# Kernel optimization log

Measured on AMD Instinct MI355X. Metric: run time of the kernel, lower is better.

Reference implementation:

```python
import jax, jax.numpy as jnp
import numpy as np


def setup_inputs() -> dict:
    key = jax.random.key(0)
    ks = jax.random.split(key, 8)
    N, C, H, W = 4, 128, 64, 64
    x = jax.random.normal(ks[0], (N, C, H, W), dtype=jnp.float32)
    s = 1.0 / np.sqrt(C)
    wq = jax.random.normal(ks[1], (C, C), dtype=jnp.float32) * s
    bq = jax.random.normal(ks[2], (C,), dtype=jnp.float32) * 0.01
    wk = jax.random.normal(ks[3], (C, C), dtype=jnp.float32) * s
    bk = jax.random.normal(ks[4], (C,), dtype=jnp.float32) * 0.01
    wv = jax.random.normal(ks[5], (C, C), dtype=jnp.float32) * s
    bv = jax.random.normal(ks[6], (C,), dtype=jnp.float32) * 0.01
    gamma = jax.random.normal(ks[7], (1,), dtype=jnp.float32) * 0.1
    return {"x": x, "wq": wq, "bq": bq, "wk": wk, "bk": bk,
            "wv": wv, "bv": bv, "gamma": gamma}


def reference(x, wq, bq, wk, bk, wv, bv, gamma):
    N, C, H, W = x.shape
    xf = x.reshape(N, C, H * W)                      # [N, C, HW]
    # 1x1 convs == per-pixel channel GEMMs
    q = jnp.einsum('dc,nci->ndi', wq, xf) + bq[None, :, None]  # [N, C, HW]
    k = jnp.einsum('dc,nci->ndi', wk, xf) + bk[None, :, None]
    v = jnp.einsum('dc,nci->ndi', wv, xf) + bv[None, :, None]
    # scores[n,i,j] = sum_c q[n,c,i] * k[n,c,j]  (query^T @ key)
    scores = jnp.einsum('nci,ncj->nij', q, k)        # [N, HW, HW]
    attn = jax.nn.softmax(scores, axis=-1)
    # out[n,c,i] = sum_j v[n,c,j] * attn[n,i,j]  (value @ attn^T)
    out = jnp.einsum('ncj,nij->nci', v, attn).reshape(N, C, H, W)
    return gamma[0] * out + x
```

## Files before the change

kernel.cpp:

```cpp
#include <hip/hip_runtime.h>

#define HW 4096
#define CC 128
#define NB 4
#define NSPLIT 4
#define KEYS_PER_SPLIT (HW / NSPLIT)

typedef __bf16 bf16x8 __attribute__((ext_vector_type(8)));
typedef float floatx4 __attribute__((ext_vector_type(4)));

__device__ __forceinline__ float row_max16(float v) {
    int x;
    x = __builtin_amdgcn_update_dpp(0, __float_as_int(v), 0x128, 0xf, 0xf, false);
    v = fmaxf(v, __int_as_float(x));
    x = __builtin_amdgcn_update_dpp(0, __float_as_int(v), 0x124, 0xf, 0xf, false);
    v = fmaxf(v, __int_as_float(x));
    x = __builtin_amdgcn_update_dpp(0, __float_as_int(v), 0x122, 0xf, 0xf, false);
    v = fmaxf(v, __int_as_float(x));
    x = __builtin_amdgcn_update_dpp(0, __float_as_int(v), 0x121, 0xf, 0xf, false);
    v = fmaxf(v, __int_as_float(x));
    return v;
}
__device__ __forceinline__ float row_sum16(float v) {
    int x;
    x = __builtin_amdgcn_update_dpp(0, __float_as_int(v), 0x128, 0xf, 0xf, false);
    v += __int_as_float(x);
    x = __builtin_amdgcn_update_dpp(0, __float_as_int(v), 0x124, 0xf, 0xf, false);
    v += __int_as_float(x);
    x = __builtin_amdgcn_update_dpp(0, __float_as_int(v), 0x122, 0xf, 0xf, false);
    v += __int_as_float(x);
    x = __builtin_amdgcn_update_dpp(0, __float_as_int(v), 0x121, 0xf, 0xf, false);
    v += __int_as_float(x);
    return v;
}

__global__ __launch_bounds__(256) void wconv_kernel(
    const float* __restrict__ wq, const float* __restrict__ wk,
    const float* __restrict__ wv, __bf16* __restrict__ wb)
{
    int idx = blockIdx.x * 256 + threadIdx.x;
    int which = idx >> 14;
    int within = idx & 16383;
    const float* src = (which == 0) ? wq : (which == 1) ? wk : wv;
    wb[idx] = (__bf16)src[within];
}

__global__ __launch_bounds__(256) void proj_kernel(
    const float* __restrict__ x, const __bf16* __restrict__ wb,
    const float* __restrict__ bq, const float* __restrict__ bk,
    const float* __restrict__ bv,
    __bf16* __restrict__ qb, __bf16* __restrict__ kb, __bf16* __restrict__ vb)
{
    __shared__ char smem_raw[128 * 70 * 2];
    __bf16* Xt = reinterpret_cast<__bf16*>(smem_raw);
    __bf16* Vt = reinterpret_cast<__bf16*>(smem_raw);

    const int m   = blockIdx.x % 3;
    const int nit = blockIdx.x / 3;
    const int n   = nit >> 6;
    const int i0  = (nit & 63) << 6;
    const int t   = threadIdx.x;

    const float* xb = x + (size_t)n * CC * HW;

#pragma unroll 4
    for (int p = 0; p < 32; ++p) {
        int c  = p * 4 + (t >> 6);
        int il = t & 63;
        Xt[il * 136 + c] = (__bf16)xb[(size_t)c * HW + i0 + il];
    }
    __syncthreads();

    const int w    = t >> 6;
    const int lane = t & 63;
    const int l16  = lane & 15;
    const int quad = lane >> 4;

    bf16x8 afrag[4];
#pragma unroll
    for (int ks = 0; ks < 4; ++ks)
        afrag[ks] = *reinterpret_cast<const bf16x8*>(
            &Xt[(w * 16 + l16) * 136 + ks * 32 + quad * 8]);

    const __bf16* wm = wb + (size_t)m * CC * CC;
    const float* Bm = (m == 0) ? bq : (m == 1) ? bk : bv;

    if (m < 2) {
        __bf16* dst = (m == 0) ? qb : kb;
#pragma unroll
        for (int h = 0; h < 8; ++h) {
            int d = h * 16 + l16;
            floatx4 acc = {0.f, 0.f, 0.f, 0.f};
#pragma unroll
            for (int ks = 0; ks < 4; ++ks) {
                bf16x8 bfrag = *reinterpret_cast<const bf16x8*>(
                    wm + (size_t)d * CC + ks * 32 + quad * 8);
                acc = __builtin_amdgcn_mfma_f32_16x16x32_bf16(afrag[ks], bfrag, acc, 0, 0, 0);
            }
            float bias = Bm[d];
#pragma unroll
            for (int r = 0; r < 4; ++r) {
                int i = i0 + w * 16 + quad * 4 + r;
                dst[(size_t)n * HW * CC + (size_t)i * CC + d] = (__bf16)(acc[r] + bias);
            }
        }
    } else {
        __syncthreads();
#pragma unroll
        for (int h = 0; h < 8; ++h) {
            int d = h * 16 + l16;
            floatx4 acc = {0.f, 0.f, 0.f, 0.f};
#pragma unroll
            for (int ks = 0; ks < 4; ++ks) {
                bf16x8 bfrag = *reinterpret_cast<const bf16x8*>(
                    wm + (size_t)d * CC + ks * 32 + quad * 8);
                acc = __builtin_amdgcn_mfma_f32_16x16x32_bf16(afrag[ks], bfrag, acc, 0, 0, 0);
            }
            float bias = Bm[d];
#pragma unroll
            for (int r = 0; r < 4; ++r)
                Vt[d * 70 + w * 16 + quad * 4 + r] = (__bf16)(acc[r] + bias);
        }
        __syncthreads();
#pragma unroll 4
        for (int p = 0; p < 32; ++p) {
            int d  = p * 4 + (t >> 6);
            int il = t & 63;
            vb[((size_t)n * CC + d) * HW + i0 + il] = Vt[d * 70 + il];
        }
    }
}

#define KT_STRIDE 136
#define VT_STRIDE 72
#define PT_STRIDE 72
#define KT_BYTES (64 * KT_STRIDE * 2)
#define VT_BYTES (128 * VT_STRIDE * 2)
#define P_OFF    (KT_BYTES + VT_BYTES)
#define T_STRIDE 129

__global__ __launch_bounds__(256, 2) void attn_split_kernel(
    const __bf16* __restrict__ qb, const __bf16* __restrict__ kb,
    const __bf16* __restrict__ vb,
    float* __restrict__ opart, float* __restrict__ ml)
{
    __shared__ char smem[P_OFF + 4 * 32 * PT_STRIDE * 2];
    __bf16* Kt = reinterpret_cast<__bf16*>(smem);
    __bf16* Vt = reinterpret_cast<__bf16*>(smem + KT_BYTES);
    float*  T  = reinterpret_cast<float*>(smem);

    const int b     = blockIdx.x;
    const int n     = (b >> 1) & 3;
    const int split = (((b >> 3) & 1) << 1) | (b & 1);
    const int it    = b >> 4;
    const int i0    = it << 7;
    const int t     = threadIdx.x;
    const int w     = t >> 6;
    const int lane  = t & 63;
    const int l16   = lane & 15;
    const int quad  = lane >> 4;

    __bf16* Pw = reinterpret_cast<__bf16*>(smem + P_OFF) + w * (32 * PT_STRIDE);

    bf16x8 qfrag[2][4];
#pragma unroll
    for (int half = 0; half < 2; ++half) {
        const __bf16* qrow = qb + ((size_t)n * HW + i0 + w * 32 + half * 16 + l16) * CC;
#pragma unroll
        for (int ks = 0; ks < 4; ++ks)
            qfrag[half][ks] = *reinterpret_cast<const bf16x8*>(qrow + ks * 32 + quad * 8);
    }

    float m_i[2][4], l_i[2][4];
    floatx4 o_acc[2][8];
#pragma unroll
    for (int half = 0; half < 2; ++half) {
#pragma unroll
        for (int r = 0; r < 4; ++r) { m_i[half][r] = -1e30f; l_i[half][r] = 0.f; }
#pragma unroll
        for (int h = 0; h < 8; ++h) o_acc[half][h] = (floatx4){0.f, 0.f, 0.f, 0.f};
    }

    const __bf16* kbase = kb + (size_t)n * HW * CC;
    const __bf16* vbase = vb + (size_t)n * CC * HW;

    const int jbeg = split * KEYS_PER_SPLIT;
    const int jend = jbeg + KEYS_PER_SPLIT;

    for (int j0 = jbeg; j0 < jend; j0 += 64) {
        bf16x8 kst[4], vst[4];
        const int jr = t >> 4, ch = t & 15;
        const int cv = t >> 3, ch2 = t & 7;
#pragma unroll
        for (int p = 0; p < 4; ++p) {
            kst[p] = *reinterpret_cast<const bf16x8*>(
                kbase + (size_t)(j0 + p * 16 + jr) * CC + ch * 8);
            vst[p] = *reinterpret_cast<const bf16x8*>(
                vbase + (size_t)(p * 32 + cv) * HW + j0 + ch2 * 8);
        }
        __syncthreads();
#pragma unroll
        for (int p = 0; p < 4; ++p) {
            *reinterpret_cast<bf16x8*>(&Kt[(p * 16 + jr) * KT_STRIDE + ch * 8]) = kst[p];
            *reinterpret_cast<bf16x8*>(&Vt[(p * 32 + cv) * VT_STRIDE + ch2 * 8]) = vst[p];
        }
        __syncthreads();

        floatx4 s[2][4];
#pragma unroll
        for (int half = 0; half < 2; ++half)
#pragma unroll
            for (int g = 0; g < 4; ++g) s[half][g] = (floatx4){0.f, 0.f, 0.f, 0.f};
#pragma unroll
        for (int ks = 0; ks < 4; ++ks) {
#pragma unroll
            for (int g = 0; g < 4; ++g) {
                bf16x8 kf = *reinterpret_cast<const bf16x8*>(
                    &Kt[(g * 16 + l16) * KT_STRIDE + ks * 32 + quad * 8]);
                s[0][g] = __builtin_amdgcn_mfma_f32_16x16x32_bf16(qfrag[0][ks], kf, s[0][g], 0, 0, 0);
                s[1][g] = __builtin_amdgcn_mfma_f32_16x16x32_bf16(qfrag[1][ks], kf, s[1][g], 0, 0, 0);
            }
        }

#pragma unroll
        for (int half = 0; half < 2; ++half) {
            float alpha[4];
#pragma unroll
            for (int r = 0; r < 4; ++r) {
                float rm = fmaxf(fmaxf(s[half][0][r], s[half][1][r]),
                                 fmaxf(s[half][2][r], s[half][3][r]));
                rm = row_max16(rm);
                float mn = fmaxf(m_i[half][r], rm);
                alpha[r] = __expf(m_i[half][r] - mn);
                m_i[half][r] = mn;
            }
#pragma unroll
            for (int g = 0; g < 4; ++g)
#pragma unroll
                for (int r = 0; r < 4; ++r)
                    s[half][g][r] = __expf(s[half][g][r] - m_i[half][r]);
#pragma unroll
            for (int r = 0; r < 4; ++r) {
                float rs = s[half][0][r] + s[half][1][r] + s[half][2][r] + s[half][3][r];
                rs = row_sum16(rs);
                l_i[half][r] = l_i[half][r] * alpha[r] + rs;
            }
#pragma unroll
            for (int h = 0; h < 8; ++h)
#pragma unroll
                for (int r = 0; r < 4; ++r)
                    o_acc[half][h][r] *= alpha[r];
#pragma unroll
            for (int g = 0; g < 4; ++g)
#pragma unroll
                for (int r = 0; r < 4; ++r)
                    Pw[(half * 16 + quad * 4 + r) * PT_STRIDE + g * 16 + l16] =
                        (__bf16)s[half][g][r];
        }

        bf16x8 pfrag[2][2];
#pragma unroll
        for (int half = 0; half < 2; ++half)
#pragma unroll
            for (int tt = 0; tt < 2; ++tt)
                pfrag[half][tt] = *reinterpret_cast<const bf16x8*>(
                    Pw + (half * 16 + l16) * PT_STRIDE + tt * 32 + quad * 8);
#pragma unroll
        for (int tt = 0; tt < 2; ++tt) {
#pragma unroll
            for (int h = 0; h < 8; ++h) {
                bf16x8 vf = *reinterpret_cast<const bf16x8*>(
                    &Vt[(h * 16 + l16) * VT_STRIDE + tt * 32 + quad * 8]);
                o_acc[0][h] = __builtin_amdgcn_mfma_f32_16x16x32_bf16(pfrag[0][tt], vf, o_acc[0][h], 0, 0, 0);
                o_acc[1][h] = __builtin_amdgcn_mfma_f32_16x16x32_bf16(pfrag[1][tt], vf, o_acc[1][h], 0, 0, 0);
            }
        }
    }

    if (l16 == 0) {
#pragma unroll
        for (int half = 0; half < 2; ++half)
#pragma unroll
            for (int r = 0; r < 4; ++r) {
                int row = w * 32 + half * 16 + quad * 4 + r;
                ml[(size_t)b * 256 + row]       = m_i[half][r];
                ml[(size_t)b * 256 + 128 + row] = l_i[half][r];
            }
    }

    __syncthreads();
#pragma unroll
    for (int pass = 0; pass < 2; ++pass) {
        if ((w >> 1) == pass) {
            int rb = (w & 1) * 32;
#pragma unroll
            for (int half = 0; half < 2; ++half)
#pragma unroll
                for (int h = 0; h < 8; ++h)
#pragma unroll
                    for (int r = 0; r < 4; ++r)
                        T[(rb + half * 16 + quad * 4 + r) * T_STRIDE + h * 16 + l16] =
                            o_acc[half][h][r];
        }
        __syncthreads();
#pragma unroll 4
        for (int p = 0; p < 32; ++p) {
            int c  = p * 4 + (t >> 6);
            int ql = t & 63;
            opart[(size_t)b * 16384 + (size_t)c * 128 + pass * 64 + ql] =
                T[ql * T_STRIDE + c];
        }
        __syncthreads();
    }
}

__global__ __launch_bounds__(256) void combine_kernel(
    const float* __restrict__ opart, const float* __restrict__ ml,
    const float* __restrict__ x, const float* __restrict__ gamma,
    float* __restrict__ out)
{
    __shared__ float wsc[NSPLIT][128];

    const int b2    = blockIdx.x;
    const int cpart = b2 & 7;
    const int qt    = b2 >> 3;
    const int n     = qt >> 5;
    const int it    = qt & 31;
    const int i0    = it << 7;
    const int t     = threadIdx.x;
    const float gm  = gamma[0];

    int battn[NSPLIT];
#pragma unroll
    for (int s = 0; s < NSPLIT; ++s)
        battn[s] = (it << 4) | ((s >> 1) << 3) | (n << 1) | (s & 1);

    if (t < 128) {
        float ms[NSPLIT], ls[NSPLIT], M = -1e30f;
#pragma unroll
        for (int s = 0; s < NSPLIT; ++s) {
            ms[s] = ml[(size_t)battn[s] * 256 + t];
            ls[s] = ml[(size_t)battn[s] * 256 + 128 + t];
            M = fmaxf(M, ms[s]);
        }
        float denom = 0.f, es[NSPLIT];
#pragma unroll
        for (int s = 0; s < NSPLIT; ++s) {
            es[s] = __expf(ms[s] - M);
            denom += es[s] * ls[s];
        }
        float inv = gm / denom;
#pragma unroll
        for (int s = 0; s < NSPLIT; ++s)
            wsc[s][t] = es[s] * inv;
    }
    __syncthreads();

#pragma unroll
    for (int p = 0; p < 8; ++p) {
        int cl = p * 2 + (t >> 7);
        int q  = t & 127;
        int c  = cpart * 16 + cl;
        size_t gidx = ((size_t)n * CC + c) * HW + i0 + q;
        float acc = x[gidx];
#pragma unroll
        for (int s = 0; s < NSPLIT; ++s)
            acc += wsc[s][q] * opart[(size_t)battn[s] * 16384 + (size_t)c * 128 + q];
        out[gidx] = acc;
    }
}

extern "C" void kernel_launch(void* const* d_in, const int* in_sizes, int n_in,
                              void* d_out, int out_size, void* d_ws, size_t ws_size,
                              hipStream_t stream) {
    const float* x     = (const float*)d_in[0];
    const float* wq    = (const float*)d_in[1];
    const float* bq    = (const float*)d_in[2];
    const float* wk    = (const float*)d_in[3];
    const float* bk    = (const float*)d_in[4];
    const float* wv    = (const float*)d_in[5];
    const float* bv    = (const float*)d_in[6];
    const float* gamma = (const float*)d_in[7];
    float* out = (float*)d_out;

    char* ws = (char*)d_ws;
    const size_t qkv_sz = (size_t)NB * HW * CC * sizeof(__bf16);
    __bf16* qb = (__bf16*)(ws);
    __bf16* kb = (__bf16*)(ws + qkv_sz);
    __bf16* vb = (__bf16*)(ws + 2 * qkv_sz);
    __bf16* wb = (__bf16*)(ws + 3 * qkv_sz);
    float* opart = (float*)(ws + 3 * qkv_sz + 3 * CC * CC * sizeof(__bf16));
    float* ml    = (float*)((char*)opart + (size_t)512 * CC * 128 * sizeof(float));

    wconv_kernel<<<192, 256, 0, stream>>>(wq, wk, wv, wb);
    proj_kernel<<<768, 256, 0, stream>>>(x, wb, bq, bk, bv, qb, kb, vb);
    attn_split_kernel<<<512, 256, 0, stream>>>(qb, kb, vb, opart, ml);
    combine_kernel<<<1024, 256, 0, stream>>>(opart, ml, x, gamma, out);
}
```

Measured before the change: 163.4 us.

## Rework flash-attention inner loop: transposed MFMA, exp2 softmax, direct V loads, bf16 partials

The attention kernel now computes S^T with K as the A operand, so each lane owns a query column. Row max and sum then need only two cross-lane shuffles instead of DPP row reductions. Softmax uses exp2 with log2e folded into the Q projection, and rescaling of the accumulators is skipped when no max changes. V is read straight from global memory instead of being staged in LDS, which frees shared memory for three blocks per CU. Partial outputs are normalized and stored as bf16, halving combine traffic at some cost in precision.

```diff
diff --git a/kernel.cpp b/kernel.cpp
--- a/kernel.cpp
+++ b/kernel.cpp
@@ -2,37 +2,14 @@
 
 #define HW 4096
 #define CC 128
-#define NB 4
 #define NSPLIT 4
 #define KEYS_PER_SPLIT (HW / NSPLIT)
+#define LOG2E 1.44269504088896f
 
 typedef __bf16 bf16x8 __attribute__((ext_vector_type(8)));
+typedef __bf16 bf16x4 __attribute__((ext_vector_type(4)));
+typedef __bf16 bf16x2 __attribute__((ext_vector_type(2)));
 typedef float floatx4 __attribute__((ext_vector_type(4)));
-
-__device__ __forceinline__ float row_max16(float v) {
-    int x;
-    x = __builtin_amdgcn_update_dpp(0, __float_as_int(v), 0x128, 0xf, 0xf, false);
-    v = fmaxf(v, __int_as_float(x));
-    x = __builtin_amdgcn_update_dpp(0, __float_as_int(v), 0x124, 0xf, 0xf, false);
-    v = fmaxf(v, __int_as_float(x));
-    x = __builtin_amdgcn_update_dpp(0, __float_as_int(v), 0x122, 0xf, 0xf, false);
-    v = fmaxf(v, __int_as_float(x));
-    x = __builtin_amdgcn_update_dpp(0, __float_as_int(v), 0x121, 0xf, 0xf, false);
-    v = fmaxf(v, __int_as_float(x));
-    return v;
-}
-__device__ __forceinline__ float row_sum16(float v) {
-    int x;
-    x = __builtin_amdgcn_update_dpp(0, __float_as_int(v), 0x128, 0xf, 0xf, false);
-    v += __int_as_float(x);
-    x = __builtin_amdgcn_update_dpp(0, __float_as_int(v), 0x124, 0xf, 0xf, false);
-    v += __int_as_float(x);
-    x = __builtin_amdgcn_update_dpp(0, __float_as_int(v), 0x122, 0xf, 0xf, false);
-    v += __int_as_float(x);
-    x = __builtin_amdgcn_update_dpp(0, __float_as_int(v), 0x121, 0xf, 0xf, false);
-    v += __int_as_float(x);
-    return v;
-}
 
 __global__ __launch_bounds__(256) void wconv_kernel(
     const float* __restrict__ wq, const float* __restrict__ wk,
@@ -84,6 +61,7 @@
 
     const __bf16* wm = wb + (size_t)m * CC * CC;
     const float* Bm = (m == 0) ? bq : (m == 1) ? bk : bv;
+    const float scale = (m == 0) ? LOG2E : 1.0f;
 
     if (m < 2) {
         __bf16* dst = (m == 0) ? qb : kb;
@@ -101,7 +79,8 @@
 #pragma unroll
             for (int r = 0; r < 4; ++r) {
                 int i = i0 + w * 16 + quad * 4 + r;
-                dst[(size_t)n * HW * CC + (size_t)i * CC + d] = (__bf16)(acc[r] + bias);
+                dst[(size_t)n * HW * CC + (size_t)i * CC + d] =
+                    (__bf16)((acc[r] + bias) * scale);
             }
         }
     } else {
@@ -132,21 +111,18 @@
 }
 
 #define KT_STRIDE 136
-#define VT_STRIDE 72
+#define KT_BYTES (64 * KT_STRIDE * 2)
 #define PT_STRIDE 72
-#define KT_BYTES (64 * KT_STRIDE * 2)
-#define VT_BYTES (128 * VT_STRIDE * 2)
-#define P_OFF    (KT_BYTES + VT_BYTES)
-#define T_STRIDE 129
-
-__global__ __launch_bounds__(256, 2) void attn_split_kernel(
+#define PT_WAVE (32 * PT_STRIDE * 2)
+#define T_STRIDE 65
+
+__global__ __launch_bounds__(256, 3) void attn_split_kernel(
     const __bf16* __restrict__ qb, const __bf16* __restrict__ kb,
     const __bf16* __restrict__ vb,
-    float* __restrict__ opart, float* __restrict__ ml)
+    __bf16* __restrict__ opart, float* __restrict__ ml)
 {
-    __shared__ char smem[P_OFF + 4 * 32 * PT_STRIDE * 2];
+    __shared__ char smem[KT_BYTES + 4 * PT_WAVE];
     __bf16* Kt = reinterpret_cast<__bf16*>(smem);
-    __bf16* Vt = reinterpret_cast<__bf16*>(smem + KT_BYTES);
     float*  T  = reinterpret_cast<float*>(smem);
 
     const int b     = blockIdx.x;
@@ -160,7 +136,7 @@
     const int l16   = lane & 15;
     const int quad  = lane >> 4;
 
-    __bf16* Pw = reinterpret_cast<__bf16*>(smem + P_OFF) + w * (32 * PT_STRIDE);
+    __bf16* Pt = reinterpret_cast<__bf16*>(smem + KT_BYTES) + w * (32 * PT_STRIDE);
 
     bf16x8 qfrag[2][4];
 #pragma unroll
@@ -171,15 +147,13 @@
             qfrag[half][ks] = *reinterpret_cast<const bf16x8*>(qrow + ks * 32 + quad * 8);
     }
 
-    float m_i[2][4], l_i[2][4];
+    float m_i[2] = {-1e30f, -1e30f};
+    float l_i[2] = {0.f, 0.f};
     floatx4 o_acc[2][8];
 #pragma unroll
-    for (int half = 0; half < 2; ++half) {
-#pragma unroll
-        for (int r = 0; r < 4; ++r) { m_i[half][r] = -1e30f; l_i[half][r] = 0.f; }
+    for (int half = 0; half < 2; ++half)
 #pragma unroll
         for (int h = 0; h < 8; ++h) o_acc[half][h] = (floatx4){0.f, 0.f, 0.f, 0.f};
-    }
 
     const __bf16* kbase = kb + (size_t)n * HW * CC;
     const __bf16* vbase = vb + (size_t)n * CC * HW;
@@ -187,23 +161,18 @@
     const int jbeg = split * KEYS_PER_SPLIT;
     const int jend = jbeg + KEYS_PER_SPLIT;
 
+    const int jr = t >> 4, ch = t & 15;
+
     for (int j0 = jbeg; j0 < jend; j0 += 64) {
-        bf16x8 kst[4], vst[4];
-        const int jr = t >> 4, ch = t & 15;
-        const int cv = t >> 3, ch2 = t & 7;
-#pragma unroll
-        for (int p = 0; p < 4; ++p) {
+        bf16x8 kst[4];
+#pragma unroll
+        for (int p = 0; p < 4; ++p)
             kst[p] = *reinterpret_cast<const bf16x8*>(
                 kbase + (size_t)(j0 + p * 16 + jr) * CC + ch * 8);
-            vst[p] = *reinterpret_cast<const bf16x8*>(
-                vbase + (size_t)(p * 32 + cv) * HW + j0 + ch2 * 8);
-        }
-        __syncthreads();
-#pragma unroll
-        for (int p = 0; p < 4; ++p) {
+        __syncthreads();
+#pragma unroll
+        for (int p = 0; p < 4; ++p)
             *reinterpret_cast<bf16x8*>(&Kt[(p * 16 + jr) * KT_STRIDE + ch * 8]) = kst[p];
-            *reinterpret_cast<bf16x8*>(&Vt[(p * 32 + cv) * VT_STRIDE + ch2 * 8]) = vst[p];
-        }
         __syncthreads();
 
         floatx4 s[2][4];
@@ -217,105 +186,117 @@
             for (int g = 0; g < 4; ++g) {
                 bf16x8 kf = *reinterpret_cast<const bf16x8*>(
                     &Kt[(g * 16 + l16) * KT_STRIDE + ks * 32 + quad * 8]);
-                s[0][g] = __builtin_amdgcn_mfma_f32_16x16x32_bf16(qfrag[0][ks], kf, s[0][g], 0, 0, 0);
-                s[1][g] = __builtin_amdgcn_mfma_f32_16x16x32_bf16(qfrag[1][ks], kf, s[1][g], 0, 0, 0);
+                s[0][g] = __builtin_amdgcn_mfma_f32_16x16x32_bf16(kf, qfrag[0][ks], s[0][g], 0, 0, 0);
+                s[1][g] = __builtin_amdgcn_mfma_f32_16x16x32_bf16(kf, qfrag[1][ks], s[1][g], 0, 0, 0);
             }
         }
 
 #pragma unroll
         for (int half = 0; half < 2; ++half) {
-            float alpha[4];
-#pragma unroll
-            for (int r = 0; r < 4; ++r) {
-                float rm = fmaxf(fmaxf(s[half][0][r], s[half][1][r]),
-                                 fmaxf(s[half][2][r], s[half][3][r]));
-                rm = row_max16(rm);
-                float mn = fmaxf(m_i[half][r], rm);
-                alpha[r] = __expf(m_i[half][r] - mn);
-                m_i[half][r] = mn;
-            }
+            float rm = fmaxf(fmaxf(fmaxf(s[half][0][0], s[half][0][1]),
+                                   fmaxf(s[half][0][2], s[half][0][3])),
+                             fmaxf(fmaxf(s[half][1][0], s[half][1][1]),
+                                   fmaxf(s[half][1][2], s[half][1][3])));
+            float rm2 = fmaxf(fmaxf(fmaxf(s[half][2][0], s[half][2][1]),
+                                    fmaxf(s[half][2][2], s[half][2][3])),
+                              fmaxf(fmaxf(s[half][3][0], s[half][3][1]),
+                                    fmaxf(s[half][3][2], s[half][3][3])));
+            rm = fmaxf(rm, rm2);
+            rm = fmaxf(rm, __shfl_xor(rm, 16, 64));
+            rm = fmaxf(rm, __shfl_xor(rm, 32, 64));
+            if (__any(rm > m_i[half])) {
+                float mn = fmaxf(m_i[half], rm);
+                float alpha = exp2f(m_i[half] - mn);
+                m_i[half] = mn;
+                l_i[half] *= alpha;
+#pragma unroll
+                for (int h = 0; h < 8; ++h)
+                    o_acc[half][h] *= alpha;
+            }
+            float mi = m_i[half];
+            float rs = 0.f;
 #pragma unroll
             for (int g = 0; g < 4; ++g)
 #pragma unroll
-                for (int r = 0; r < 4; ++r)
-                    s[half][g][r] = __expf(s[half][g][r] - m_i[half][r]);
-#pragma unroll
-            for (int r = 0; r < 4; ++r) {
-                float rs = s[half][0][r] + s[half][1][r] + s[half][2][r] + s[half][3][r];
-                rs = row_sum16(rs);
-                l_i[half][r] = l_i[half][r] * alpha[r] + rs;
-            }
+                for (int r = 0; r < 4; ++r) {
+                    float e = exp2f(s[half][g][r] - mi);
+                    s[half][g][r] = e;
+                    rs += e;
+                }
+            rs += __shfl_xor(rs, 16, 64);
+            rs += __shfl_xor(rs, 32, 64);
+            l_i[half] += rs;
+
+#pragma unroll
+            for (int g = 0; g < 4; ++g) {
+                bf16x4 pk = {(__bf16)s[half][g][0], (__bf16)s[half][g][1],
+                             (__bf16)s[half][g][2], (__bf16)s[half][g][3]};
+                *reinterpret_cast<bf16x4*>(
+                    &Pt[(half * 16 + l16) * PT_STRIDE + g * 16 + quad * 4]) = pk;
+            }
+        }
+
+#pragma unroll
+        for (int tt = 0; tt < 2; ++tt) {
+            bf16x8 vf[8];
 #pragma unroll
             for (int h = 0; h < 8; ++h)
-#pragma unroll
-                for (int r = 0; r < 4; ++r)
-                    o_acc[half][h][r] *= alpha[r];
-#pragma unroll
-            for (int g = 0; g < 4; ++g)
-#pragma unroll
-                for (int r = 0; r < 4; ++r)
-                    Pw[(half * 16 + quad * 4 + r) * PT_STRIDE + g * 16 + l16] =
-                        (__bf16)s[half][g][r];
-        }
-
-        bf16x8 pfrag[2][2];
-#pragma unroll
-        for (int half = 0; half < 2; ++half)
-#pragma unroll
-            for (int tt = 0; tt < 2; ++tt)
-                pfrag[half][tt] = *reinterpret_cast<const bf16x8*>(
-                    Pw + (half * 16 + l16) * PT_STRIDE + tt * 32 + quad * 8);
-#pragma unroll
-        for (int tt = 0; tt < 2; ++tt) {
+                vf[h] = *reinterpret_cast<const bf16x8*>(
+                    vbase + (size_t)(h * 16 + l16) * HW + j0 + tt * 32 + quad * 8);
+            bf16x8 pf0 = *reinterpret_cast<const bf16x8*>(
+                &Pt[l16 * PT_STRIDE + tt * 32 + quad * 8]);
+            bf16x8 pf1 = *reinterpret_cast<const bf16x8*>(
+                &Pt[(16 + l16) * PT_STRIDE + tt * 32 + quad * 8]);
 #pragma unroll
             for (int h = 0; h < 8; ++h) {
-                bf16x8 vf = *reinterpret_cast<const bf16x8*>(
-                    &Vt[(h * 16 + l16) * VT_STRIDE + tt * 32 + quad * 8]);
-                o_acc[0][h] = __builtin_amdgcn_mfma_f32_16x16x32_bf16(pfrag[0][tt], vf, o_acc[0][h], 0, 0, 0);
-                o_acc[1][h] = __builtin_amdgcn_mfma_f32_16x16x32_bf16(pfrag[1][tt], vf, o_acc[1][h], 0, 0, 0);
-            }
-        }
-    }
-
-    if (l16 == 0) {
-#pragma unroll
-        for (int half = 0; half < 2; ++half)
-#pragma unroll
-            for (int r = 0; r < 4; ++r) {
-                int row = w * 32 + half * 16 + quad * 4 + r;
-                ml[(size_t)b * 256 + row]       = m_i[half][r];
-                ml[(size_t)b * 256 + 128 + row] = l_i[half][r];
-            }
-    }
+                o_acc[0][h] = __builtin_amdgcn_mfma_f32_16x16x32_bf16(vf[h], pf0, o_acc[0][h], 0, 0, 0);
+                o_acc[1][h] = __builtin_amdgcn_mfma_f32_16x16x32_bf16(vf[h], pf1, o_acc[1][h], 0, 0, 0);
+            }
+        }
+    }
+
+    if (quad == 0) {
+#pragma unroll
+        for (int half = 0; half < 2; ++half) {
+            int q = w * 32 + half * 16 + l16;
+            ml[(size_t)b * 256 + q]       = m_i[half];
+            ml[(size_t)b * 256 + 128 + q] = l_i[half];
+        }
+    }
+
+    float inv[2] = {1.f / l_i[0], 1.f / l_i[1]};
 
     __syncthreads();
 #pragma unroll
     for (int pass = 0; pass < 2; ++pass) {
         if ((w >> 1) == pass) {
-            int rb = (w & 1) * 32;
+            int ql = (w & 1) * 32;
 #pragma unroll
             for (int half = 0; half < 2; ++half)
 #pragma unroll
                 for (int h = 0; h < 8; ++h)
 #pragma unroll
                     for (int r = 0; r < 4; ++r)
-                        T[(rb + half * 16 + quad * 4 + r) * T_STRIDE + h * 16 + l16] =
-                            o_acc[half][h][r];
+                        T[(h * 16 + quad * 4 + r) * T_STRIDE + ql + half * 16 + l16] =
+                            o_acc[half][h][r] * inv[half];
         }
         __syncthreads();
 #pragma unroll 4
-        for (int p = 0; p < 32; ++p) {
-            int c  = p * 4 + (t >> 6);
-            int ql = t & 63;
-            opart[(size_t)b * 16384 + (size_t)c * 128 + pass * 64 + ql] =
-                T[ql * T_STRIDE + c];
+        for (int p = 0; p < 16; ++p) {
+            int c  = p * 8 + (t >> 5);
+            int q2 = (t & 31) * 2;
+            float f0 = T[c * T_STRIDE + q2];
+            float f1 = T[c * T_STRIDE + q2 + 1];
+            bf16x2 pk = {(__bf16)f0, (__bf16)f1};
+            *reinterpret_cast<bf16x2*>(
+                &opart[(size_t)b * 16384 + (size_t)c * 128 + pass * 64 + q2]) = pk;
         }
         __syncthreads();
     }
 }
 
 __global__ __launch_bounds__(256) void combine_kernel(
-    const float* __restrict__ opart, const float* __restrict__ ml,
+    const __bf16* __restrict__ opart, const float* __restrict__ ml,
     const float* __restrict__ x, const float* __restrict__ gamma,
     float* __restrict__ out)
 {
@@ -346,7 +327,7 @@
         float denom = 0.f, es[NSPLIT];
 #pragma unroll
         for (int s = 0; s < NSPLIT; ++s) {
-            es[s] = __expf(ms[s] - M);
+            es[s] = exp2f(ms[s] - M);
             denom += es[s] * ls[s];
         }
         float inv = gm / denom;
@@ -357,16 +338,21 @@
     __syncthreads();
 
 #pragma unroll
-    for (int p = 0; p < 8; ++p) {
-        int cl = p * 2 + (t >> 7);
-        int q  = t & 127;
-        int c  = cpart * 16 + cl;
-        size_t gidx = ((size_t)n * CC + c) * HW + i0 + q;
-        float acc = x[gidx];
-#pragma unroll
-        for (int s = 0; s < NSPLIT; ++s)
-            acc += wsc[s][q] * opart[(size_t)battn[s] * 16384 + (size_t)c * 128 + q];
-        out[gidx] = acc;
+    for (int p = 0; p < 4; ++p) {
+        int c  = cpart * 16 + p * 4 + (t >> 6);
+        int q2 = (t & 63) * 2;
+        size_t gidx = ((size_t)n * CC + c) * HW + i0 + q2;
+        float2 xv = *reinterpret_cast<const float2*>(&x[gidx]);
+        float a0 = xv.x, a1 = xv.y;
+#pragma unroll
+        for (int s = 0; s < NSPLIT; ++s) {
+            bf16x2 ov = *reinterpret_cast<const bf16x2*>(
+                &opart[(size_t)battn[s] * 16384 + (size_t)c * 128 + q2]);
+            a0 += wsc[s][q2]     * (float)ov[0];
+            a1 += wsc[s][q2 + 1] * (float)ov[1];
+        }
+        float2 o2 = {a0, a1};
+        *reinterpret_cast<float2*>(&out[gidx]) = o2;
     }
 }
 
@@ -384,13 +370,13 @@
     float* out = (float*)d_out;
 
     char* ws = (char*)d_ws;
-    const size_t qkv_sz = (size_t)NB * HW * CC * sizeof(__bf16);
+    const size_t qkv_sz = (size_t)4 * HW * CC * sizeof(__bf16);
     __bf16* qb = (__bf16*)(ws);
     __bf16* kb = (__bf16*)(ws + qkv_sz);
     __bf16* vb = (__bf16*)(ws + 2 * qkv_sz);
     __bf16* wb = (__bf16*)(ws + 3 * qkv_sz);
-    float* opart = (float*)(ws + 3 * qkv_sz + 3 * CC * CC * sizeof(__bf16));
-    float* ml    = (float*)((char*)opart + (size_t)512 * CC * 128 * sizeof(float));
+    __bf16* opart = (__bf16*)(ws + 3 * qkv_sz + 3 * CC * CC * sizeof(__bf16));
+    float* ml = (float*)((char*)opart + (size_t)512 * 16384 * sizeof(__bf16));
 
     wconv_kernel<<<192, 256, 0, stream>>>(wq, wk, wv, wb);
     proj_kernel<<<768, 256, 0, stream>>>(x, wb, bq, bk, bv, qb, kb, vb);
```

Result: slower. 192.7 us (+18.0%).
